# Kernel tuning notes

Hardware: AMD Instinct MI355X
Metric: run time of the kernel (lower is better)

The kernel has to match this reference:

```python
import jax, jax.numpy as jnp
import numpy as np


def setup_inputs() -> dict:
    key = jax.random.key(0)
    kq, kk, kv, km = jax.random.split(key, 4)
    b, h, s, d = 4, 16, 2048, 64
    q = jax.random.normal(kq, (b, h, s, d), dtype=jnp.float32)
    k = jax.random.normal(kk, (b, h, s, d), dtype=jnp.float32)
    v = jax.random.normal(kv, (b, h, s, d), dtype=jnp.float32)
    # True = attend (keep), False = masked out (matches torch semantics where
    # ~attention_mask marks positions to fill with -min)
    attention_mask = jax.random.randint(km, (b, s), 0, 2).astype(jnp.bool_)
    return {"q": q, "k": k, "v": v, "attention_mask": attention_mask}


def reference(q, k, v, attention_mask):
    # scaled dot-product attention: softmax(q k^T / sqrt(d)) v
    scale = q.shape[-1] ** (-0.5)
    sim = jnp.einsum("bhid,bhjd->bhij", q, k) * scale  # (b,h,s,s)
    neg = jnp.finfo(sim.dtype).min
    # mask broadcast (b,1,1,s): keep where True, fill with finfo.min where False
    sim = jnp.where(attention_mask[:, None, None, :], sim, neg)
    attn = jax.nn.softmax(sim, axis=-1)
    return jnp.einsum("bhij,bhjd->bhid", attn, v)
```

## Files before the change

kernel.cpp:

```cpp
#include <hip/hip_runtime.h>
#include <hip/hip_bf16.h>

typedef __attribute__((ext_vector_type(8))) short short8;
typedef __attribute__((ext_vector_type(4))) float floatx4;

constexpr int B = 4, H = 16, S = 2048, D = 64;
constexpr int BM = 64;
constexpr int BN = 64;
constexpr int LDK = 72;

#define QSCALE (0.125f * 1.44269504088896f)

__device__ __forceinline__ short f2bf(float x) {
  __hip_bfloat16 h = __float2bfloat16(x);
  return *reinterpret_cast<short*>(&h);
}

__device__ __forceinline__ short8 ld8f_bf(const float* p, float sc) {
  floatx4 a = *(const floatx4*)p;
  floatx4 b = *(const floatx4*)(p + 4);
  union { short8 s; __hip_bfloat162 h[4]; } u;
  u.h[0] = __float22bfloat162_rn(make_float2(a[0] * sc, a[1] * sc));
  u.h[1] = __float22bfloat162_rn(make_float2(a[2] * sc, a[3] * sc));
  u.h[2] = __float22bfloat162_rn(make_float2(b[0] * sc, b[1] * sc));
  u.h[3] = __float22bfloat162_rn(make_float2(b[2] * sc, b[3] * sc));
  return u.s;
}

__global__ __launch_bounds__(256, 2)
void attn_flash_kernel(const float* __restrict__ Q, const float* __restrict__ Kp,
                       const float* __restrict__ Vp, const int* __restrict__ Mask,
                       float* __restrict__ Out) {
  __shared__ __align__(16) short ks[2][BN * LDK];
  __shared__ __align__(16) short vs[2][D * 64];
  __shared__ __align__(16) short ps[4][16 * LDK];
  __shared__ int ms[2][BN];

  const int t = threadIdx.x;
  const int wave = t >> 6;
  const int lane = t & 63;
  const int quad = lane >> 4;
  const int lm = lane & 15;

  const int bh = blockIdx.y;
  const int bb = bh >> 4;
  const int mblk = blockIdx.x;

  const float* Qb = Q + (size_t)bh * S * D;
  const float* Kb = Kp + (size_t)bh * S * D;
  const float* Vb = Vp + (size_t)bh * S * D;
  const int* Mb = Mask + bb * S;

  const int qrow = mblk * BM + wave * 16 + lm;
  const float* qp = Qb + (size_t)qrow * D;
  const short8 qf0 = ld8f_bf(qp + 0 * 32 + quad * 8, QSCALE);
  const short8 qf1 = ld8f_bf(qp + 1 * 32 + quad * 8, QSCALE);

  short8 ones;
#pragma unroll
  for (int j = 0; j < 8; ++j) ones[j] = (short)0x3F80;

  floatx4 acc[4], accl;
#pragma unroll
  for (int d = 0; d < 4; ++d) acc[d] = (floatx4){0.f, 0.f, 0.f, 0.f};
  accl = (floatx4){0.f, 0.f, 0.f, 0.f};

  const int r0 = t >> 3;
  const int c0 = t & 7;
  const int r1 = r0 + 32;
  const float* kp0 = Kb + (size_t)r0 * D + c0 * 8;
  const float* kp1 = Kb + (size_t)r1 * D + c0 * 8;
  const float* vp0 = Vb + (size_t)r0 * D + c0 * 8;
  const float* vp1 = Vb + (size_t)r1 * D + c0 * 8;

  floatx4 kr[2][2], vr[2][2];
  int mreg = 0;

  auto stage_load = [&](int kb) {
    const size_t off = (size_t)kb * D;
    kr[0][0] = *(const floatx4*)(kp0 + off);
    kr[0][1] = *(const floatx4*)(kp0 + off + 4);
    kr[1][0] = *(const floatx4*)(kp1 + off);
    kr[1][1] = *(const floatx4*)(kp1 + off + 4);
    vr[0][0] = *(const floatx4*)(vp0 + off);
    vr[0][1] = *(const floatx4*)(vp0 + off + 4);
    vr[1][0] = *(const floatx4*)(vp1 + off);
    vr[1][1] = *(const floatx4*)(vp1 + off + 4);
    if (t < BN) mreg = Mb[kb + t];
  };

  auto stage_write = [&](int buf) {
    if (t < BN) ms[buf][t] = mreg;
#pragma unroll
    for (int it = 0; it < 2; ++it) {
      const int r = it ? r1 : r0;
      floatx4 a = kr[it][0], b = kr[it][1];
      union { short8 s; __hip_bfloat162 h[4]; } u;
      u.h[0] = __float22bfloat162_rn(make_float2(a[0], a[1]));
      u.h[1] = __float22bfloat162_rn(make_float2(a[2], a[3]));
      u.h[2] = __float22bfloat162_rn(make_float2(b[0], b[1]));
      u.h[3] = __float22bfloat162_rn(make_float2(b[2], b[3]));
      *(short8*)&ks[buf][r * LDK + c0 * 8] = u.s;
      floatx4 va = vr[it][0], vb2 = vr[it][1];
      const int r3 = r >> 3, r7 = r & 7;
#pragma unroll
      for (int j = 0; j < 4; ++j)
        vs[buf][(c0 * 8 + j) * 64 + ((r3 ^ c0 ^ j) & 7) * 8 + r7] = f2bf(va[j]);
#pragma unroll
      for (int j = 0; j < 4; ++j)
        vs[buf][(c0 * 8 + 4 + j) * 64 + ((r3 ^ c0 ^ (4 + j)) & 7) * 8 + r7] = f2bf(vb2[j]);
    }
  };

  stage_load(0);
  stage_write(0);

  int cur = 0;
  for (int kb = 0; kb < S; kb += BN) {
    __syncthreads();
    const bool hn = (kb + BN) < S;
    if (hn) stage_load(kb + BN);

    const short* ksc = ks[cur];
    const short* vsc = vs[cur];
    const int* msc = ms[cur];

    floatx4 sc[4];
    __builtin_amdgcn_s_setprio(1);
#pragma unroll
    for (int nt = 0; nt < 4; ++nt) {
      short8 kf0 = *(const short8*)&ksc[(nt * 16 + lm) * LDK + 0 * 32 + quad * 8];
      short8 kf1 = *(const short8*)&ksc[(nt * 16 + lm) * LDK + 1 * 32 + quad * 8];
      floatx4 z = (floatx4){0.f, 0.f, 0.f, 0.f};
      z = __builtin_amdgcn_mfma_f32_16x16x32_bf16(qf0, kf0, z, 0, 0, 0);
      z = __builtin_amdgcn_mfma_f32_16x16x32_bf16(qf1, kf1, z, 0, 0, 0);
      sc[nt] = z;
    }
    __builtin_amdgcn_s_setprio(0);

    float s_el[4][4];
#pragma unroll
    for (int nt = 0; nt < 4; ++nt) {
      int keep = msc[nt * 16 + lm];
#pragma unroll
      for (int r = 0; r < 4; ++r)
        s_el[nt][r] = keep ? __builtin_exp2f(sc[nt][r]) : 0.0f;
    }

    short* pw = &ps[wave][0];
#pragma unroll
    for (int nt = 0; nt < 4; ++nt)
#pragma unroll
      for (int r = 0; r < 4; ++r)
        pw[(quad * 4 + r) * LDK + nt * 16 + lm] = f2bf(s_el[nt][r]);

    __builtin_amdgcn_s_setprio(1);
#pragma unroll
    for (int kt = 0; kt < 2; ++kt) {
      short8 af = *(const short8*)&pw[lm * LDK + kt * 32 + quad * 8];
      accl = __builtin_amdgcn_mfma_f32_16x16x32_bf16(af, ones, accl, 0, 0, 0);
#pragma unroll
      for (int dn = 0; dn < 4; ++dn) {
        const int drow = dn * 16 + lm;
        const int dswz = ((dn * 2 + (lm >> 3)) ^ (lm & 7)) & 7;
        short8 bf = *(const short8*)&vsc[drow * 64 + (((kt * 4 + quad) ^ dswz) & 7) * 8];
        acc[dn] = __builtin_amdgcn_mfma_f32_16x16x32_bf16(af, bf, acc[dn], 0, 0, 0);
      }
    }
    __builtin_amdgcn_s_setprio(0);

    if (hn) stage_write(cur ^ 1);
    cur ^= 1;
  }

#pragma unroll
  for (int r = 0; r < 4; ++r) {
    float inv = 1.0f / accl[r];
    int row = mblk * BM + wave * 16 + quad * 4 + r;
    float* op = Out + (size_t)(bh * S + row) * D;
#pragma unroll
    for (int dn = 0; dn < 4; ++dn)
      op[dn * 16 + lm] = acc[dn][r] * inv;
  }
}

extern "C" void kernel_launch(void* const* d_in, const int* in_sizes, int n_in,
                              void* d_out, int out_size, void* d_ws, size_t ws_size,
                              hipStream_t stream) {
  const float* q = (const float*)d_in[0];
  const float* k = (const float*)d_in[1];
  const float* v = (const float*)d_in[2];
  const int* mask = (const int*)d_in[3];
  float* out = (float*)d_out;
  dim3 grid(S / BM, B * H);
  attn_flash_kernel<<<grid, dim3(256), 0, stream>>>(q, k, v, mask, out);
}
```

Before: 288.2 us.

## Transpose QK MFMA operands and vectorize P/V shared-memory stores

Swaps the A/B operands of the QK^T MFMA so each lane holds scores for consecutive keys of one query row. The P tile can then be written to LDS with packed 64-bit stores instead of scalar bf16 stores, and mask values are read as int4. V is now loaded with a new thread mapping so pairs of adjacent keys are packed into 32-bit transposed LDS writes with a simpler XOR swizzle. The goal is fewer LDS store instructions and less conversion overhead, at the risk of changed bank-conflict patterns and less coalesced V global loads.

```diff
diff --git a/kernel.cpp b/kernel.cpp
--- a/kernel.cpp
+++ b/kernel.cpp
@@ -8,13 +8,9 @@
 constexpr int BM = 64;
 constexpr int BN = 64;
 constexpr int LDK = 72;
+constexpr int LDP = 72;
 
 #define QSCALE (0.125f * 1.44269504088896f)
-
-__device__ __forceinline__ short f2bf(float x) {
-  __hip_bfloat16 h = __float2bfloat16(x);
-  return *reinterpret_cast<short*>(&h);
-}
 
 __device__ __forceinline__ short8 ld8f_bf(const float* p, float sc) {
   floatx4 a = *(const floatx4*)p;
@@ -27,14 +23,19 @@
   return u.s;
 }
 
+__device__ __forceinline__ unsigned pk2(float lo, float hi) {
+  __hip_bfloat162 h = __float22bfloat162_rn(make_float2(lo, hi));
+  return *reinterpret_cast<unsigned*>(&h);
+}
+
 __global__ __launch_bounds__(256, 2)
 void attn_flash_kernel(const float* __restrict__ Q, const float* __restrict__ Kp,
                        const float* __restrict__ Vp, const int* __restrict__ Mask,
                        float* __restrict__ Out) {
   __shared__ __align__(16) short ks[2][BN * LDK];
   __shared__ __align__(16) short vs[2][D * 64];
-  __shared__ __align__(16) short ps[4][16 * LDK];
-  __shared__ int ms[2][BN];
+  __shared__ __align__(16) short ps[4][16 * LDP];
+  __shared__ __align__(16) int ms[2][BN];
 
   const int t = threadIdx.x;
   const int wave = t >> 6;
@@ -68,24 +69,26 @@
   const int r0 = t >> 3;
   const int c0 = t & 7;
   const int r1 = r0 + 32;
-  const float* kp0 = Kb + (size_t)r0 * D + c0 * 8;
-  const float* kp1 = Kb + (size_t)r1 * D + c0 * 8;
-  const float* vp0 = Vb + (size_t)r0 * D + c0 * 8;
-  const float* vp1 = Vb + (size_t)r1 * D + c0 * 8;
+  const int kp = t & 31;
+  const int cv = t >> 5;
+  const float* kg0 = Kb + (size_t)r0 * D + c0 * 8;
+  const float* kg1 = Kb + (size_t)r1 * D + c0 * 8;
+  const float* vg0 = Vb + (size_t)(2 * kp) * D + cv * 8;
+  const float* vg1 = Vb + (size_t)(2 * kp + 1) * D + cv * 8;
 
   floatx4 kr[2][2], vr[2][2];
   int mreg = 0;
 
   auto stage_load = [&](int kb) {
     const size_t off = (size_t)kb * D;
-    kr[0][0] = *(const floatx4*)(kp0 + off);
-    kr[0][1] = *(const floatx4*)(kp0 + off + 4);
-    kr[1][0] = *(const floatx4*)(kp1 + off);
-    kr[1][1] = *(const floatx4*)(kp1 + off + 4);
-    vr[0][0] = *(const floatx4*)(vp0 + off);
-    vr[0][1] = *(const floatx4*)(vp0 + off + 4);
-    vr[1][0] = *(const floatx4*)(vp1 + off);
-    vr[1][1] = *(const floatx4*)(vp1 + off + 4);
+    kr[0][0] = *(const floatx4*)(kg0 + off);
+    kr[0][1] = *(const floatx4*)(kg0 + off + 4);
+    kr[1][0] = *(const floatx4*)(kg1 + off);
+    kr[1][1] = *(const floatx4*)(kg1 + off + 4);
+    vr[0][0] = *(const floatx4*)(vg0 + off);
+    vr[0][1] = *(const floatx4*)(vg0 + off + 4);
+    vr[1][0] = *(const floatx4*)(vg1 + off);
+    vr[1][1] = *(const floatx4*)(vg1 + off + 4);
     if (t < BN) mreg = Mb[kb + t];
   };
 
@@ -101,14 +104,13 @@
       u.h[2] = __float22bfloat162_rn(make_float2(b[0], b[1]));
       u.h[3] = __float22bfloat162_rn(make_float2(b[2], b[3]));
       *(short8*)&ks[buf][r * LDK + c0 * 8] = u.s;
-      floatx4 va = vr[it][0], vb2 = vr[it][1];
-      const int r3 = r >> 3, r7 = r & 7;
-#pragma unroll
-      for (int j = 0; j < 4; ++j)
-        vs[buf][(c0 * 8 + j) * 64 + ((r3 ^ c0 ^ j) & 7) * 8 + r7] = f2bf(va[j]);
-#pragma unroll
-      for (int j = 0; j < 4; ++j)
-        vs[buf][(c0 * 8 + 4 + j) * 64 + ((r3 ^ c0 ^ (4 + j)) & 7) * 8 + r7] = f2bf(vb2[j]);
+    }
+#pragma unroll
+    for (int j = 0; j < 4; ++j) {
+      *(unsigned*)&vs[buf][(cv * 8 + j) * 64 + ((2 * kp) ^ (j << 3))] =
+          pk2(vr[0][0][j], vr[1][0][j]);
+      *(unsigned*)&vs[buf][(cv * 8 + 4 + j) * 64 + ((2 * kp) ^ ((4 + j) << 3))] =
+          pk2(vr[0][1][j], vr[1][1][j]);
     }
   };
 
@@ -132,8 +134,8 @@
       short8 kf0 = *(const short8*)&ksc[(nt * 16 + lm) * LDK + 0 * 32 + quad * 8];
       short8 kf1 = *(const short8*)&ksc[(nt * 16 + lm) * LDK + 1 * 32 + quad * 8];
       floatx4 z = (floatx4){0.f, 0.f, 0.f, 0.f};
-      z = __builtin_amdgcn_mfma_f32_16x16x32_bf16(qf0, kf0, z, 0, 0, 0);
-      z = __builtin_amdgcn_mfma_f32_16x16x32_bf16(qf1, kf1, z, 0, 0, 0);
+      z = __builtin_amdgcn_mfma_f32_16x16x32_bf16(kf0, qf0, z, 0, 0, 0);
+      z = __builtin_amdgcn_mfma_f32_16x16x32_bf16(kf1, qf1, z, 0, 0, 0);
       sc[nt] = z;
     }
     __builtin_amdgcn_s_setprio(0);
@@ -141,29 +143,31 @@
     float s_el[4][4];
 #pragma unroll
     for (int nt = 0; nt < 4; ++nt) {
-      int keep = msc[nt * 16 + lm];
+      int4 mm = *(const int4*)&msc[nt * 16 + quad * 4];
+      int mv[4] = {mm.x, mm.y, mm.z, mm.w};
 #pragma unroll
       for (int r = 0; r < 4; ++r)
-        s_el[nt][r] = keep ? __builtin_exp2f(sc[nt][r]) : 0.0f;
+        s_el[nt][r] = mv[r] ? __builtin_exp2f(sc[nt][r]) : 0.0f;
     }
 
     short* pw = &ps[wave][0];
 #pragma unroll
-    for (int nt = 0; nt < 4; ++nt)
-#pragma unroll
-      for (int r = 0; r < 4; ++r)
-        pw[(quad * 4 + r) * LDK + nt * 16 + lm] = f2bf(s_el[nt][r]);
+    for (int nt = 0; nt < 4; ++nt) {
+      uint2 pp = make_uint2(pk2(s_el[nt][0], s_el[nt][1]),
+                            pk2(s_el[nt][2], s_el[nt][3]));
+      *(uint2*)&pw[lm * LDP + nt * 16 + quad * 4] = pp;
+    }
 
     __builtin_amdgcn_s_setprio(1);
+    const int vswz = (lm & 7) << 3;
 #pragma unroll
     for (int kt = 0; kt < 2; ++kt) {
-      short8 af = *(const short8*)&pw[lm * LDK + kt * 32 + quad * 8];
+      short8 af = *(const short8*)&pw[lm * LDP + kt * 32 + quad * 8];
       accl = __builtin_amdgcn_mfma_f32_16x16x32_bf16(af, ones, accl, 0, 0, 0);
 #pragma unroll
       for (int dn = 0; dn < 4; ++dn) {
-        const int drow = dn * 16 + lm;
-        const int dswz = ((dn * 2 + (lm >> 3)) ^ (lm & 7)) & 7;
-        short8 bf = *(const short8*)&vsc[drow * 64 + (((kt * 4 + quad) ^ dswz) & 7) * 8];
+        short8 bf = *(const short8*)&vsc[(dn * 16 + lm) * 64 +
+                                         ((kt * 32 + quad * 8) ^ vswz)];
         acc[dn] = __builtin_amdgcn_mfma_f32_16x16x32_bf16(af, bf, acc[dn], 0, 0, 0);
       }
     }
```

Measured after the change: 294.0 us. +2.0%, slower.
